# Optimization experiments

Hardware: AMD Instinct MI355X
Metric: run time of the kernel (lower is better)

The kernel has to match this reference:

```python
import jax, jax.numpy as jnp
import numpy as np

B, H, G, N, D = 1, 32, 64, 128, 128   # batch, heads, blocks, block_len, head_dim
S = 256                               # sketch dim (multiple of 16)
BIT_PACK = 8


def setup_inputs() -> dict:
    key = jax.random.key(0)
    k1, k2, k3 = jax.random.split(key, 3)
    data = jax.random.normal(k1, (B, H, G, N, D), dtype=jnp.float32)
    # binary per-channel outlier mask, float {0,1}, shape matches data.shape[:3] + (D,)
    outlier_mask = jax.random.randint(k2, (B, H, G, D), 0, 2).astype(jnp.float32)
    # proj_dir_quant = proj_dir_score.T -> shape (S, D)
    proj_dir_quant = jax.random.normal(k3, (S, D), dtype=jnp.float32)
    return {"data": data, "outlier_mask": outlier_mask, "proj_dir_quant": proj_dir_quant}


def _pack_bits(sketch):
    # sketch: (..., S). Reshape to (..., S//8, 8), threshold at 0, pack sign bits into uint8.
    x = sketch.reshape(*sketch.shape[:-1], -1, BIT_PACK)
    enc = (2 ** jnp.arange(BIT_PACK, dtype=jnp.int32))  # [1,2,4,...,128]
    packed = ((x > 0).astype(jnp.int32) * enc).sum(axis=-1)  # max 255, fits uint8
    return packed.astype(jnp.uint8)


def reference(data, outlier_mask, proj_dir_quant):
    s = proj_dir_quant.shape[0]
    m = outlier_mask[..., None, :]                     # (B,H,G,1,D) broadcast over tokens
    key_outlier = data * m
    key_inlier = data * (1.0 - m)
    # '...nd,sd->...ns' : sign-random-projection sketch
    sk_outlier = jnp.einsum('bhgnd,sd->bhgns', key_outlier, proj_dir_quant)
    sk_inlier = jnp.einsum('bhgnd,sd->bhgns', key_inlier, proj_dir_quant)
    hash_inlier = _pack_bits(sk_inlier)                # (B,H,G,N,S//8)
    hash_outlier = _pack_bits(sk_outlier)[..., : s // 16]  # (B,H,G,N,S//16)
    return (hash_inlier, hash_outlier)
```

## Files before the change

### kernel.cpp

```cpp
#include <hip/hip_runtime.h>

#define NB_HG 2048
#define DIM_N 128
#define DIM_D 128
#define DIM_S 256
#define PH 16
#define BSW 128


__global__ void transpose_proj_kernel(const float* __restrict__ proj,
                                      float* __restrict__ projT)
{
    const int d = blockIdx.x;
    const int s = threadIdx.x;
    projT[d * DIM_S + s] = proj[s * DIM_D + d];
}

template<bool TP>
__global__ __launch_bounds__(256)
void qjl_sketch_kernel(const float* __restrict__ data,
                       const float* __restrict__ mask,
                       const float* __restrict__ pmat,
                       int* __restrict__ out)
{
    __shared__ float Xt[2][PH * DIM_N];
    __shared__ float Bs[2][PH * BSW];
    __shared__ int   cidx[DIM_D];
    __shared__ int   wcnt[2];

    const int type = blockIdx.x;
    const int hg   = blockIdx.y;
    const int tid  = threadIdx.x;

    bool sel = false; int pos = 0, w = 0;
    if (tid < 128) {
        const float m = mask[hg * DIM_D + tid];
        sel = (type == 2) ? (m != 0.0f) : (m == 0.0f);
        const unsigned long long bal = __ballot(sel);
        const int lane = tid & 63;
        w = tid >> 6;
        if (lane == 0) wcnt[w] = __popcll(bal);
        pos = __popcll(bal & ((1ull << lane) - 1ull));
    }
    __syncthreads();
    if (sel) cidx[pos + (w ? wcnt[0] : 0)] = tid;
    __syncthreads();
    const int K = wcnt[0] + wcnt[1];

    const int tn = tid & 15;
    const int ts = tid >> 4;
    const int C0 = 4 * tn;
    const int sl = ts * 8;
    const int sbase = (type == 1) ? 128 : 0;

    float acc[8][8];
    #pragma unroll
    for (int j = 0; j < 8; ++j)
        #pragma unroll
        for (int i = 0; i < 8; ++i) acc[j][i] = 0.0f;

    const int cl_s  = tid & 15;
    const int nh    = tid >> 4;
    const int pcs_s = 4 * (cl_s & 7);

    float4 xr[2], br[2];

    auto LOADR = [&](int base, int kp) {
        if (cl_s < kp) {
            const int dg = cidx[base + cl_s];
            const float* Xs = data + (size_t)hg * (DIM_N * DIM_D) + dg;
            #pragma unroll
            for (int g = 0; g < 2; ++g) {
                const int n0 = nh * 8 + g * 4;
                xr[g].x = Xs[(size_t)(n0 + 0) * DIM_D];
                xr[g].y = Xs[(size_t)(n0 + 1) * DIM_D];
                xr[g].z = Xs[(size_t)(n0 + 2) * DIM_D];
                xr[g].w = Xs[(size_t)(n0 + 3) * DIM_D];
            }
            if (TP) {
                const float* Ps = pmat + (size_t)dg * DIM_S + sbase;
                #pragma unroll
                for (int g = 0; g < 2; ++g)
                    br[g] = *reinterpret_cast<const float4*>(Ps + nh * 8 + g * 4);
            } else {
                #pragma unroll
                for (int g = 0; g < 2; ++g) {
                    const int s0l = nh * 8 + g * 4;
                    br[g].x = pmat[(size_t)(sbase + s0l + 0) * DIM_D + dg];
                    br[g].y = pmat[(size_t)(sbase + s0l + 1) * DIM_D + dg];
                    br[g].z = pmat[(size_t)(sbase + s0l + 2) * DIM_D + dg];
                    br[g].w = pmat[(size_t)(sbase + s0l + 3) * DIM_D + dg];
                }
            }
        }
    };
    auto WRITER = [&](int b, int kp) {
        if (cl_s < kp) {
            float* xrow = &Xt[b][cl_s * DIM_N];
            float* brow = &Bs[b][cl_s * BSW];
            #pragma unroll
            for (int g = 0; g < 2; ++g) {
                const int n0 = nh * 8 + g * 4;
                *reinterpret_cast<float4*>(&xrow[n0 ^ pcs_s]) = xr[g];
                *reinterpret_cast<float4*>(&brow[n0 ^ pcs_s]) = br[g];
            }
        }
    };

    auto COMPUTE = [&](int b, int kp) {
        const float* Xb = Xt[b];
        const float* Bb = Bs[b];
        #pragma unroll 8
        for (int cl = 0; cl < kp; ++cl) {
            const int pcs = 4 * (cl & 7);
            const int pA  = sl ^ pcs;
            const float4 bA = *reinterpret_cast<const float4*>(&Bb[cl * BSW + pA]);
            const float4 bB = *reinterpret_cast<const float4*>(&Bb[cl * BSW + (pA ^ 4)]);
            const int P = C0 ^ pcs;
            const float4 q0 = *reinterpret_cast<const float4*>(&Xb[cl * DIM_N + P]);
            const float4 q1 = *reinterpret_cast<const float4*>(&Xb[cl * DIM_N + P + 64]);

            #pragma unroll
            for (int j = 0; j < 8; ++j) {
                const float bv = (j == 0) ? bA.x : (j == 1) ? bA.y : (j == 2) ? bA.z
                               : (j == 3) ? bA.w : (j == 4) ? bB.x : (j == 5) ? bB.y
                               : (j == 6) ? bB.z : bB.w;
                acc[j][0] = fmaf(bv, q0.x, acc[j][0]);
                acc[j][1] = fmaf(bv, q0.y, acc[j][1]);
                acc[j][2] = fmaf(bv, q0.z, acc[j][2]);
                acc[j][3] = fmaf(bv, q0.w, acc[j][3]);
                acc[j][4] = fmaf(bv, q1.x, acc[j][4]);
                acc[j][5] = fmaf(bv, q1.y, acc[j][5]);
                acc[j][6] = fmaf(bv, q1.z, acc[j][6]);
                acc[j][7] = fmaf(bv, q1.w, acc[j][7]);
            }
        }
    };

    {
        const int kp0 = (K < PH) ? K : PH;
        LOADR(0, kp0);
        WRITER(0, kp0);
        __syncthreads();
    }
    int b = 0;
    for (int base = 0; base < K; base += PH, b ^= 1) {
        const int kpc = (K - base < PH) ? (K - base) : PH;
        const int nb  = base + PH;
        const int kpn = (nb < K) ? ((K - nb < PH) ? (K - nb) : PH) : 0;
        if (kpn) LOADR(nb, kpn);
        COMPUTE(b, kpc);
        if (kpn) {
            WRITER(b ^ 1, kpn);
            __syncthreads();
        }
    }

    const size_t inl_total = (size_t)NB_HG * DIM_N * 32;
    #pragma unroll
    for (int i = 0; i < 8; ++i) {
        int byte = 0;
        #pragma unroll
        for (int j = 0; j < 8; ++j)
            if (acc[j][i] > 0.0f) byte |= (1 << j);
        const int n = (i < 4) ? (C0 + i) : (64 + C0 + (i - 4));
        size_t idx;
        if (type == 2)
            idx = inl_total + ((size_t)hg * DIM_N + n) * 16 + ts;
        else
            idx = ((size_t)hg * DIM_N + n) * 32 + (type == 1 ? 16 : 0) + ts;
        out[idx] = byte;
    }
}

extern "C" void kernel_launch(void* const* d_in, const int* in_sizes, int n_in,
                              void* d_out, int out_size, void* d_ws, size_t ws_size,
                              hipStream_t stream) {
    const float* data = (const float*)d_in[0];
    const float* mask = (const float*)d_in[1];
    const float* proj = (const float*)d_in[2];
    int* out = (int*)d_out;

    dim3 grid(3, NB_HG);
    const size_t tp_bytes = (size_t)DIM_D * DIM_S * sizeof(float);
    if (ws_size >= tp_bytes) {
        float* projT = (float*)d_ws;
        transpose_proj_kernel<<<DIM_D, DIM_S, 0, stream>>>(proj, projT);
        qjl_sketch_kernel<true><<<grid, 256, 0, stream>>>(data, mask, projT, out);
    } else {
        qjl_sketch_kernel<false><<<grid, 256, 0, stream>>>(data, mask, proj, out);
    }
}
```

Before: 203.0 us.

## Stage data and projection tiles via direct global-to-LDS DMA loads

Replaces the register-staged double-buffer loads (global to VGPR, then LDS store) with `__builtin_amdgcn_global_load_lds` DMA. It uses 4-byte gathers for the data columns and 16-byte loads for transposed projection rows. The XOR swizzle is moved onto source addresses, and a tail clamp on the channel index replaces per-lane predicates. The aim is to cut VGPR pressure and the extra LDS write instructions, and to overlap the next tile's fetch with compute. The risks are that the barrier may not wait for the outstanding DMA loads, and that the tail clamp reads `cidx[K-1]`, which is out of range when K is zero.

```diff
diff --git a/kernel.cpp b/kernel.cpp
--- a/kernel.cpp
+++ b/kernel.cpp
@@ -7,6 +7,16 @@
 #define PH 16
 #define BSW 128
 
+
+typedef const __attribute__((address_space(1))) void* gas_t;
+typedef __attribute__((address_space(3))) void* las_t;
+
+__device__ __forceinline__ void dma4(const float* g, float* l) {
+    __builtin_amdgcn_global_load_lds((gas_t)g, (las_t)l, 4, 0, 0);
+}
+__device__ __forceinline__ void dma16(const float* g, float* l) {
+    __builtin_amdgcn_global_load_lds((gas_t)g, (las_t)l, 16, 0, 0);
+}
 
 __global__ void transpose_proj_kernel(const float* __restrict__ proj,
                                       float* __restrict__ projT)
@@ -59,57 +69,55 @@
         #pragma unroll
         for (int i = 0; i < 8; ++i) acc[j][i] = 0.0f;
 
-    const int cl_s  = tid & 15;
-    const int nh    = tid >> 4;
-    const int pcs_s = 4 * (cl_s & 7);
+    const int l  = tid & 63;
+    const int wv = tid >> 6;
+    const float* Xg = data + (size_t)hg * (DIM_N * DIM_D);
 
-    float4 xr[2], br[2];
-
-    auto LOADR = [&](int base, int kp) {
-        if (cl_s < kp) {
-            const int dg = cidx[base + cl_s];
-            const float* Xs = data + (size_t)hg * (DIM_N * DIM_D) + dg;
+    auto ISSUE = [&](int base, int bb) {
+        #pragma unroll
+        for (int r = 0; r < 4; ++r) {
+            const int cl  = wv * 4 + r;
+            const int src = base + cl;
+            const int dg  = cidx[src < K ? src : K - 1];
+            const int pcs = 4 * (cl & 7);
             #pragma unroll
-            for (int g = 0; g < 2; ++g) {
-                const int n0 = nh * 8 + g * 4;
-                xr[g].x = Xs[(size_t)(n0 + 0) * DIM_D];
-                xr[g].y = Xs[(size_t)(n0 + 1) * DIM_D];
-                xr[g].z = Xs[(size_t)(n0 + 2) * DIM_D];
-                xr[g].w = Xs[(size_t)(n0 + 3) * DIM_D];
+            for (int h = 0; h < 2; ++h) {
+                const int n = h * 64 + (l ^ pcs);
+                dma4(Xg + (size_t)n * DIM_D + dg, &Xt[bb][cl * DIM_N + h * 64]);
             }
-            if (TP) {
-                const float* Ps = pmat + (size_t)dg * DIM_S + sbase;
+        }
+        if (TP) {
+            #pragma unroll
+            for (int rr = 0; rr < 2; ++rr) {
+                const int cl0  = wv * 4 + rr * 2;
+                const int row  = cl0 + (l >> 5);
+                const int src  = base + row;
+                const int dg   = cidx[src < K ? src : K - 1];
+                const int pcsr = 4 * (row & 7);
+                const int c4   = 4 * (l & 31);
+                dma16(pmat + (size_t)dg * DIM_S + sbase + (c4 ^ pcsr),
+                      &Bs[bb][cl0 * BSW]);
+            }
+        } else {
+            #pragma unroll
+            for (int r = 0; r < 4; ++r) {
+                const int cl  = wv * 4 + r;
+                const int src = base + cl;
+                const int dg  = cidx[src < K ? src : K - 1];
+                const int pcs = 4 * (cl & 7);
                 #pragma unroll
-                for (int g = 0; g < 2; ++g)
-                    br[g] = *reinterpret_cast<const float4*>(Ps + nh * 8 + g * 4);
-            } else {
-                #pragma unroll
-                for (int g = 0; g < 2; ++g) {
-                    const int s0l = nh * 8 + g * 4;
-                    br[g].x = pmat[(size_t)(sbase + s0l + 0) * DIM_D + dg];
-                    br[g].y = pmat[(size_t)(sbase + s0l + 1) * DIM_D + dg];
-                    br[g].z = pmat[(size_t)(sbase + s0l + 2) * DIM_D + dg];
-                    br[g].w = pmat[(size_t)(sbase + s0l + 3) * DIM_D + dg];
+                for (int h = 0; h < 2; ++h) {
+                    const int s_l = h * 64 + (l ^ pcs);
+                    dma4(pmat + (size_t)(sbase + s_l) * DIM_D + dg,
+                         &Bs[bb][cl * BSW + h * 64]);
                 }
             }
         }
     };
-    auto WRITER = [&](int b, int kp) {
-        if (cl_s < kp) {
-            float* xrow = &Xt[b][cl_s * DIM_N];
-            float* brow = &Bs[b][cl_s * BSW];
-            #pragma unroll
-            for (int g = 0; g < 2; ++g) {
-                const int n0 = nh * 8 + g * 4;
-                *reinterpret_cast<float4*>(&xrow[n0 ^ pcs_s]) = xr[g];
-                *reinterpret_cast<float4*>(&brow[n0 ^ pcs_s]) = br[g];
-            }
-        }
-    };
 
-    auto COMPUTE = [&](int b, int kp) {
-        const float* Xb = Xt[b];
-        const float* Bb = Bs[b];
+    auto COMPUTE = [&](int bb, int kp) {
+        const float* Xb = Xt[bb];
+        const float* Bb = Bs[bb];
         #pragma unroll 8
         for (int cl = 0; cl < kp; ++cl) {
             const int pcs = 4 * (cl & 7);
@@ -137,23 +145,16 @@
         }
     };
 
-    {
-        const int kp0 = (K < PH) ? K : PH;
-        LOADR(0, kp0);
-        WRITER(0, kp0);
-        __syncthreads();
-    }
+    ISSUE(0, 0);
+    __syncthreads();
+
     int b = 0;
     for (int base = 0; base < K; base += PH, b ^= 1) {
-        const int kpc = (K - base < PH) ? (K - base) : PH;
-        const int nb  = base + PH;
-        const int kpn = (nb < K) ? ((K - nb < PH) ? (K - nb) : PH) : 0;
-        if (kpn) LOADR(nb, kpn);
+        const int kpc  = (K - base < PH) ? (K - base) : PH;
+        const bool nxt = (base + PH < K);
+        if (nxt) ISSUE(base + PH, b ^ 1);
         COMPUTE(b, kpc);
-        if (kpn) {
-            WRITER(b ^ 1, kpn);
-            __syncthreads();
-        }
+        if (nxt) __syncthreads();
     }
 
     const size_t inl_total = (size_t)NB_HG * DIM_N * 32;
```

Measured after the change: 204.6 us. No clear change (+0.8%).
